# Kernel optimization log

Measured on AMD Instinct MI355X. Metric: run time of the kernel, lower is better.

Reference implementation:

```python
import jax, jax.numpy as jnp
import numpy as np

N, K, A, LOCAL, PAIR = 1024, 48, 5, 512, 128
RBF_BINS = 16

def _normalize(v, eps=1e-8):
    return v / jnp.sqrt(jnp.sum(v * v, axis=-1, keepdims=True) + eps)

def _frames(pos):
    # pos: (N, A, 3); backbone frame from N(0), CA(1), C(2) via Gram-Schmidt
    n, ca, c = pos[:, 0], pos[:, 1], pos[:, 2]
    e1 = _normalize(c - ca)
    v2 = n - ca
    e2 = _normalize(v2 - jnp.sum(v2 * e1, -1, keepdims=True) * e1)
    e3 = jnp.cross(e1, e2)
    R = jnp.stack([e1, e2, e3], axis=-1)  # (N,3,3) columns are frame axes
    return R, ca

def _rbf(d, d_min=0.0, d_max=22.0, bins=RBF_BINS):
    centers = jnp.linspace(d_min, d_max, bins)
    step = (d_max - d_min) / bins
    return jnp.exp(-((d[..., None] - centers) / step) ** 2)

def setup_inputs():
    key = jax.random.key(0)
    ks = jax.random.split(key, 16)
    def rn(k, shape, scale=1.0):
        return (scale * jax.random.normal(k, shape)).astype(jnp.float32)
    local = rn(ks[0], (N, LOCAL))
    pos = rn(ks[1], (N, A, 3), 3.0)
    pair = rn(ks[2], (N, N, PAIR), 0.1)
    neighbours = jax.random.randint(ks[3], (N, K), 0, N).astype(jnp.int32)
    mask = jnp.ones((N,), dtype=bool)
    d_dist = A * A * RBF_BINS   # 400
    d_dir = A * A * 3           # 75
    d_vec = 2 * A * 3           # 30
    s = lambda f: 1.0 / np.sqrt(f)
    return dict(
        local=local, pos=pos, pair=pair, neighbours=neighbours, mask=mask,
        W_li=rn(ks[4], (LOCAL, PAIR), s(LOCAL)),
        W_lj=rn(ks[5], (LOCAL, PAIR), s(LOCAL)),
        W_dist=rn(ks[6], (d_dist, PAIR), s(d_dist)),
        W_dir=rn(ks[7], (d_dir, PAIR), s(d_dir)),
        W_rot=rn(ks[8], (9, PAIR), s(9)),
        W_vec=rn(ks[9], (d_vec, PAIR), s(d_vec)),
        ln_scale=jnp.ones((PAIR,), jnp.float32),
        ln_bias=jnp.zeros((PAIR,), jnp.float32),
        mlp_w1=rn(ks[10], (PAIR, 2 * PAIR), s(PAIR)),
        mlp_b1=jnp.zeros((2 * PAIR,), jnp.float32),
        mlp_w2=rn(ks[11], (2 * PAIR, PAIR), s(2 * PAIR)),
        mlp_b2=jnp.zeros((PAIR,), jnp.float32),
    )

def reference(local, pos, pair, neighbours, mask,
              W_li, W_lj, W_dist, W_dir, W_rot, W_vec,
              ln_scale, ln_bias, mlp_w1, mlp_b1, mlp_w2, mlp_b2):
    n_idx = jnp.arange(neighbours.shape[0])
    pair_mask = (mask[:, None] & mask[neighbours]) & (neighbours != -1)
    p = pair[n_idx[:, None], neighbours]                      # (N,K,PAIR) gather
    R, t = _frames(pos)                                       # (N,3,3), (N,3)
    pos_nb = pos[neighbours]                                  # (N,K,A,3)
    # source / target node feature projections
    p = p + (local @ W_li)[:, None] + (local @ W_lj)[neighbours]
    # distance features: all atom-pair distances, RBF-encoded in [0, 22]
    off = pos[:, None, :, None, :] - pos_nb[:, :, None, :, :] # (N,K,A,A,3)
    dist = jnp.sqrt(jnp.sum(off * off, -1) + 1e-8)            # (N,K,A,A)
    p = p + _rbf(dist).reshape(*neighbours.shape, -1) @ W_dist
    # direction features: atom-pair offsets in the local frame, normalized
    off_local = jnp.einsum('nij,nkabi->nkabj', R, off)
    p = p + _normalize(off_local).reshape(*neighbours.shape, -1) @ W_dir
    # relative rotation features: R_i^T R_j, flattened
    R_rel = jnp.einsum('nai,nkaj->nkij', R, R[neighbours])
    p = p + R_rel.reshape(*neighbours.shape, 9) @ W_rot
    # pair vector features: self and neighbour atoms in the local frame (x0.1)
    x_self = jnp.einsum('nij,nai->naj', R, pos - t[:, None])            # (N,A,3)
    x_nb = jnp.einsum('nij,nkai->nkaj', R, pos_nb - t[:, None, None])   # (N,K,A,3)
    vec = jnp.concatenate(
        (0.1 * jnp.broadcast_to(x_self[:, None], x_nb.shape), 0.1 * x_nb),
        axis=-1).reshape(*neighbours.shape, -1)
    p = p + vec @ W_vec
    # LayerNorm (scale + offset)
    mu = jnp.mean(p, -1, keepdims=True)
    var = jnp.var(p, -1, keepdims=True)
    p = (p - mu) * jax.lax.rsqrt(var + 1e-5) * ln_scale + ln_bias
    # MLP: hidden 2*PAIR, gelu, linear out
    p = jax.nn.gelu(p @ mlp_w1 + mlp_b1) @ mlp_w2 + mlp_b2
    return p, pair_mask
```

## Files before the change

kernel.cpp:

```cpp
#include <hip/hip_runtime.h>
#include <hip/hip_bf16.h>
#include <math.h>

#define N 1024
#define K 48
#define A 5
#define LOCALD 512
#define PAIRD 128
#define ROWS 32
#define FEATK 544
#define SF_STRIDE_B 1152

#define WS_LI (N*9 + N*3 + N*15)
#define WS_LJ (WS_LI + N*128)
#define WCT_OFF 1159168u
#define W1T_OFF 1298432u
#define W2T_OFF 1363968u
#define PA_OFF  1429504u
#define WS_NEEDED (1429504ull + 49152ull*128*2)

typedef _Float16 half8 __attribute__((ext_vector_type(8)));
typedef float f32x16 __attribute__((ext_vector_type(16)));

__device__ __forceinline__ float gelu_fast(float x) {
    float u2 = 1.5957691216057308f * x * (1.0f + 0.044715f * x * x);
    float t = __expf(-u2);
    return x * __builtin_amdgcn_rcpf(1.0f + t);
}

__device__ __forceinline__ void frame_from(const float* __restrict__ P, float* __restrict__ R) {
    float e1x = P[6] - P[3], e1y = P[7] - P[4], e1z = P[8] - P[5];
    float inv1 = rsqrtf(e1x * e1x + e1y * e1y + e1z * e1z + 1e-8f);
    e1x *= inv1; e1y *= inv1; e1z *= inv1;
    float v2x = P[0] - P[3], v2y = P[1] - P[4], v2z = P[2] - P[5];
    float dp = v2x * e1x + v2y * e1y + v2z * e1z;
    float e2x = v2x - dp * e1x, e2y = v2y - dp * e1y, e2z = v2z - dp * e1z;
    float inv2 = rsqrtf(e2x * e2x + e2y * e2y + e2z * e2z + 1e-8f);
    e2x *= inv2; e2y *= inv2; e2z *= inv2;
    float e3x = e1y * e2z - e1z * e2y;
    float e3y = e1z * e2x - e1x * e2z;
    float e3z = e1x * e2y - e1y * e2x;
    R[0] = e1x; R[1] = e2x; R[2] = e3x;
    R[3] = e1y; R[4] = e2y; R[5] = e3y;
    R[6] = e1z; R[7] = e2z; R[8] = e3z;
}

__global__ __launch_bounds__(256) void prep_kernel(
    const float* __restrict__ local_,
    const float* __restrict__ W_li, const float* __restrict__ W_lj,
    const float* __restrict__ Wd, const float* __restrict__ Wdir,
    const float* __restrict__ Wrot, const float* __restrict__ Wv,
    const float* __restrict__ w1, const float* __restrict__ w2,
    float* __restrict__ ws, char* __restrict__ wsb)
{
    const int tid = threadIdx.x;
    if (blockIdx.x >= 256) {
        _Float16* wct = (_Float16*)(wsb + WCT_OFF);
        _Float16* w1t = (_Float16*)(wsb + W1T_OFF);
        _Float16* w2t = (_Float16*)(wsb + W2T_OFF);
        int g = (blockIdx.x - 256) * 256 + tid;
        if (g < 128 * 544) {
            int c = g & 127, f = g >> 7;
            float v = 0.0f;
            if (f < 400) v = Wd[(size_t)f * 128 + c];
            else if (f < 475) v = Wdir[(size_t)(f - 400) * 128 + c];
            else if (f < 484) v = Wrot[(size_t)(f - 475) * 128 + c];
            else if (f < 514) v = Wv[(size_t)(f - 484) * 128 + c];
            wct[(size_t)c * FEATK + f] = (_Float16)v;
        } else {
            int g2 = g - 128 * 544;
            if (g2 < 256 * 128) {
                int c = g2 & 255, f = g2 >> 8;
                w1t[(size_t)c * 128 + f] = (_Float16)w1[(size_t)f * 256 + c];
            } else {
                int g3 = g2 - 256 * 128;
                if (g3 < 128 * 256) {
                    int c = g3 & 127, f = g3 >> 7;
                    w2t[(size_t)c * 256 + f] = (_Float16)w2[(size_t)f * 128 + c];
                }
            }
        }
        return;
    }

    const int n0 = blockIdx.x * 4;
    __shared__ float sl[4][LOCALD];
    for (int t = tid; t < 4 * LOCALD; t += 256) {
        int r = t >> 9, q = t & 511;
        sl[r][q] = local_[(size_t)(n0 + r) * LOCALD + q];
    }
    __syncthreads();

    const int c = tid & 127;
    const int hh = tid >> 7;
    const int r0 = hh * 2;
    float ali0 = 0, ali1 = 0, alj0 = 0, alj1 = 0;
    const float* wli = W_li + c;
    const float* wlj = W_lj + c;
    #pragma unroll 8
    for (int f = 0; f < LOCALD; ++f) {
        float a_ = wli[(size_t)f * 128];
        float b_ = wlj[(size_t)f * 128];
        float l0 = sl[r0 + 0][f], l1 = sl[r0 + 1][f];
        ali0 += l0 * a_; ali1 += l1 * a_;
        alj0 += l0 * b_; alj1 += l1 * b_;
    }
    ws[WS_LI + (size_t)(n0 + r0 + 0) * 128 + c] = ali0;
    ws[WS_LI + (size_t)(n0 + r0 + 1) * 128 + c] = ali1;
    ws[WS_LJ + (size_t)(n0 + r0 + 0) * 128 + c] = alj0;
    ws[WS_LJ + (size_t)(n0 + r0 + 1) * 128 + c] = alj1;
}

__device__ __forceinline__ void sfw(char* smem, int r, int f, float v) {
    int off = r * SF_STRIDE_B + ((f * 2) ^ ((r & 7) << 4));
    *(_Float16*)(smem + off) = (_Float16)v;
}

template<bool SPLIT>
__global__ __launch_bounds__(256, 4) void main_kernel(
    const float* __restrict__ pair, const float* __restrict__ pos,
    const int* __restrict__ neigh, const int* __restrict__ mask,
    const float* __restrict__ ln_s, const float* __restrict__ ln_b,
    const float* __restrict__ b1, const float* __restrict__ b2,
    const float* __restrict__ ws, const char* __restrict__ wsb,
    _Float16* __restrict__ pa, float* __restrict__ out)
{
    const int R0 = blockIdx.x * ROWS;
    const int tid = threadIdx.x;
    const int lane = tid & 63;
    const int wv = tid >> 6;
    const int myrow = lane & 31;
    const int hi = lane >> 5;
    const int khalf = hi * 8;
    const int swz = (myrow & 7) << 4;

    __shared__ __align__(16) char smem[40960];
    int*   sn  = (int*)(smem + 36864);
    int*   sj  = (int*)(smem + 36992);
    float* spn = (float*)(smem + 37120);
    float* spj = (float*)(smem + 39040);

    const _Float16* wct = (const _Float16*)(wsb + WCT_OFF);
    const int colbase = wv * 32 + myrow;

    if (tid < ROWS) {
        int Rg = R0 + tid;
        int n = Rg / K;
        int kk = Rg - n * K;
        int j = neigh[n * K + kk];
        if (j < 0) j += N;
        sn[tid] = n; sj[tid] = j;
    }
    __syncthreads();

    const int nb0 = R0 / K;
    const int nb1 = (nb0 + 1 < N) ? nb0 + 1 : nb0;
    float li0 = ws[WS_LI + (size_t)nb0 * PAIRD + colbase];
    float li1 = ws[WS_LI + (size_t)nb1 * PAIRD + colbase];
    float pv[16];
    #pragma unroll
    for (int q = 0; q < 16; ++q) {
        int rr = (q & 3) + 8 * (q >> 2) + 4 * hi;
        int nq = sn[rr], jq = sj[rr];
        float li = (nq == nb0) ? li0 : li1;
        pv[q] = __builtin_nontemporal_load(&pair[((size_t)nq * N + jq) * PAIRD + colbase])
              + ws[WS_LJ + (size_t)jq * PAIRD + colbase] + li;
    }

    for (int t = tid; t < ROWS * 15; t += 256) {
        int r = t / 15, q = t % 15;
        spn[t] = pos[(size_t)sn[r] * 15 + q];
        spj[t] = pos[(size_t)sj[r] * 15 + q];
    }
    __syncthreads();

    {
        const int fr  = tid >> 3;
        const int sub = tid & 7;
        const float* Pn = spn + fr * 15;
        const float* Pj = spj + fr * 15;

        sfw(smem, fr, 514 + sub, 0.0f);
        sfw(smem, fr, 522 + sub, 0.0f);
        sfw(smem, fr, 530 + sub, 0.0f);
        if (sub < 6) sfw(smem, fr, 538 + sub, 0.0f);

        float rn[9];
        frame_from(Pn, rn);

        #pragma unroll
        for (int m = 0; m < 4; ++m) {
            int ab = sub + 8 * m;
            if (ab < 25) {
                int a = ab / 5, b = ab - 5 * (ab / 5);
                float o0 = Pn[a * 3 + 0] - Pj[b * 3 + 0];
                float o1 = Pn[a * 3 + 1] - Pj[b * 3 + 1];
                float o2 = Pn[a * 3 + 2] - Pj[b * 3 + 2];
                float d = sqrtf(o0 * o0 + o1 * o1 + o2 * o2 + 1e-8f);
                float z = d * (16.0f / 22.0f);
                int base = a * 80 + b * 16;
                int rb = fr * SF_STRIDE_B;
                int rsw = (fr & 7) << 4;
                #pragma unroll
                for (int bp = 0; bp < 8; ++bp) {
                    float e0 = __expf(-z * z);
                    float z1 = z - 1.0666666666666667f;
                    float e1 = __expf(-z1 * z1);
                    z = z1 - 1.0666666666666667f;
                    union { _Float16 h[2]; unsigned u; } pk;
                    pk.h[0] = (_Float16)e0; pk.h[1] = (_Float16)e1;
                    int off = rb + (((base + bp * 2) * 2) ^ rsw);
                    *(unsigned*)(smem + off) = pk.u;
                }
                float l0 = rn[0] * o0 + rn[3] * o1 + rn[6] * o2;
                float l1 = rn[1] * o0 + rn[4] * o1 + rn[7] * o2;
                float l2 = rn[2] * o0 + rn[5] * o1 + rn[8] * o2;
                float inv = rsqrtf(l0 * l0 + l1 * l1 + l2 * l2 + 1e-8f);
                int dbase = 400 + a * 15 + b * 3;
                sfw(smem, fr, dbase + 0, l0 * inv);
                sfw(smem, fr, dbase + 1, l1 * inv);
                sfw(smem, fr, dbase + 2, l2 * inv);
            }
        }

        #pragma unroll
        for (int m = 0; m < 2; ++m) {
            int task = (m == 0) ? sub : (sub < 2 ? 8 + sub : -1);
            if (task >= 0) {
                int a = task >> 1;
                int kind = task & 1;
                const float* Ps = kind ? Pj : Pn;
                float v0 = Ps[a * 3 + 0] - Pn[3];
                float v1 = Ps[a * 3 + 1] - Pn[4];
                float v2 = Ps[a * 3 + 2] - Pn[5];
                float x0 = rn[0] * v0 + rn[3] * v1 + rn[6] * v2;
                float x1 = rn[1] * v0 + rn[4] * v1 + rn[7] * v2;
                float x2 = rn[2] * v0 + rn[5] * v1 + rn[8] * v2;
                int dbase = 484 + a * 6 + kind * 3;
                sfw(smem, fr, dbase + 0, 0.1f * x0);
                sfw(smem, fr, dbase + 1, 0.1f * x1);
                sfw(smem, fr, dbase + 2, 0.1f * x2);
            }
        }

        if (sub == 7) {
            float rj[9];
            frame_from(Pj, rj);
            #pragma unroll
            for (int i = 0; i < 3; ++i)
                #pragma unroll
                for (int jd = 0; jd < 3; ++jd) {
                    float v = rn[0 * 3 + i] * rj[0 * 3 + jd]
                            + rn[1 * 3 + i] * rj[1 * 3 + jd]
                            + rn[2 * 3 + i] * rj[2 * 3 + jd];
                    sfw(smem, fr, 475 + i * 3 + jd, v);
                }
        }
    }
    __syncthreads();

    f32x16 acc0, acc1;
    #pragma unroll
    for (int q = 0; q < 16; ++q) { acc0[q] = 0.0f; acc1[q] = 0.0f; }
    {
        const _Float16* wp = wct + (size_t)colbase * FEATK + khalf;
        #pragma unroll
        for (int ks = 0; ks < 34; ks += 2) {
            half8 b0 = *(const half8*)(wp + ks * 16);
            half8 b1 = *(const half8*)(wp + (ks + 1) * 16);
            int k0 = ks * 16 + khalf;
            int k1 = (ks + 1) * 16 + khalf;
            half8 a0 = *(const half8*)(smem + myrow * SF_STRIDE_B + ((k0 * 2) ^ swz));
            half8 a1 = *(const half8*)(smem + myrow * SF_STRIDE_B + ((k1 * 2) ^ swz));
            acc0 = __builtin_amdgcn_mfma_f32_32x32x16_f16(a0, b0, acc0, 0, 0, 0);
            acc1 = __builtin_amdgcn_mfma_f32_32x32x16_f16(a1, b1, acc1, 0, 0, 0);
        }
    }
    __syncthreads();

    #pragma unroll
    for (int q = 0; q < 16; ++q) {
        int rr = (q & 3) + 8 * (q >> 2) + 4 * hi;
        *(float*)(smem + rr * 512 + colbase * 4) = acc0[q] + acc1[q] + pv[q];
    }
    __syncthreads();

    {
        float lns0 = ln_s[lane], lns1 = ln_s[lane + 64];
        float lnb0 = ln_b[lane], lnb1 = ln_b[lane + 64];
        #pragma unroll
        for (int rr8 = 0; rr8 < 8; ++rr8) {
            int row = wv * 8 + rr8;
            float v0 = *(float*)(smem + row * 512 + lane * 4);
            float v1 = *(float*)(smem + row * 512 + (lane + 64) * 4);
            float s = v0 + v1, s2 = v0 * v0 + v1 * v1;
            #pragma unroll
            for (int o = 32; o > 0; o >>= 1) {
                s += __shfl_xor(s, o, 64);
                s2 += __shfl_xor(s2, o, 64);
            }
            float mu = s * (1.0f / 128.0f);
            float var = s2 * (1.0f / 128.0f) - mu * mu;
            float rs = rsqrtf(var + 1e-5f);
            float y0 = (v0 - mu) * rs * lns0 + lnb0;
            float y1 = (v1 - mu) * rs * lns1 + lnb1;
            if constexpr (SPLIT) {
                pa[(size_t)(R0 + row) * PAIRD + lane]      = (_Float16)y0;
                pa[(size_t)(R0 + row) * PAIRD + lane + 64] = (_Float16)y1;
            } else {
                int sw = (row & 7) << 4;
                *(_Float16*)(smem + 16384 + row * 256 + ((lane * 2) ^ sw)) = (_Float16)y0;
                *(_Float16*)(smem + 16384 + row * 256 + (((lane + 64) * 2) ^ sw)) = (_Float16)y1;
            }
        }
    }
    if constexpr (SPLIT) return;

    __syncthreads();

    {
        const _Float16* w1t = (const _Float16*)(wsb + W1T_OFF);
        const int c0 = wv * 64 + myrow;
        const int c1 = c0 + 32;
        const _Float16* wp0 = w1t + (size_t)c0 * 128 + khalf;
        const _Float16* wp1 = w1t + (size_t)c1 * 128 + khalf;
        f32x16 h0, h1;
        #pragma unroll
        for (int q = 0; q < 16; ++q) { h0[q] = 0.0f; h1[q] = 0.0f; }
        #pragma unroll
        for (int ks = 0; ks < 8; ++ks) {
            half8 wf0 = *(const half8*)(wp0 + ks * 16);
            half8 wf1 = *(const half8*)(wp1 + ks * 16);
            int k0 = ks * 16 + khalf;
            half8 a = *(const half8*)(smem + 16384 + myrow * 256 + ((k0 * 2) ^ swz));
            h0 = __builtin_amdgcn_mfma_f32_32x32x16_f16(a, wf0, h0, 0, 0, 0);
            h1 = __builtin_amdgcn_mfma_f32_32x32x16_f16(a, wf1, h1, 0, 0, 0);
        }
        float bb0 = b1[c0], bb1 = b1[c1];
        #pragma unroll
        for (int q = 0; q < 16; ++q) {
            int rr = (q & 3) + 8 * (q >> 2) + 4 * hi;
            int sw = (rr & 7) << 4;
            *(_Float16*)(smem + rr * 512 + ((c0 * 2) ^ sw)) = (_Float16)gelu_fast(h0[q] + bb0);
            *(_Float16*)(smem + rr * 512 + ((c1 * 2) ^ sw)) = (_Float16)gelu_fast(h1[q] + bb1);
        }
    }
    __syncthreads();

    {
        const _Float16* w2t = (const _Float16*)(wsb + W2T_OFF);
        const int oc = wv * 32 + myrow;
        const _Float16* wp = w2t + (size_t)oc * 256 + khalf;
        f32x16 o0, o1;
        #pragma unroll
        for (int q = 0; q < 16; ++q) { o0[q] = 0.0f; o1[q] = 0.0f; }
        #pragma unroll
        for (int ks = 0; ks < 16; ks += 2) {
            half8 w0 = *(const half8*)(wp + ks * 16);
            half8 w1f = *(const half8*)(wp + (ks + 1) * 16);
            int k0 = ks * 16 + khalf;
            int k1 = (ks + 1) * 16 + khalf;
            half8 a0 = *(const half8*)(smem + myrow * 512 + ((k0 * 2) ^ swz));
            half8 a1 = *(const half8*)(smem + myrow * 512 + ((k1 * 2) ^ swz));
            o0 = __builtin_amdgcn_mfma_f32_32x32x16_f16(a0, w0, o0, 0, 0, 0);
            o1 = __builtin_amdgcn_mfma_f32_32x32x16_f16(a1, w1f, o1, 0, 0, 0);
        }
        float bb = b2[oc];
        #pragma unroll
        for (int q = 0; q < 16; ++q) {
            int rr = (q & 3) + 8 * (q >> 2) + 4 * hi;
            __builtin_nontemporal_store(o0[q] + o1[q] + bb,
                &out[((size_t)(R0 + rr)) * PAIRD + oc]);
        }
    }

    if (tid < ROWS) {
        int Rg = R0 + tid;
        int n = Rg / K;
        int kk = Rg - n * K;
        int jr = neigh[n * K + kk];
        int jj = jr < 0 ? jr + N : jr;
        bool pm = (jr != -1) && (mask[n] != 0) && (mask[jj] != 0);
        out[(size_t)N * K * PAIRD + Rg] = pm ? 1.0f : 0.0f;
    }
}

__global__ __launch_bounds__(256, 3) void mlp_kernel(
    const _Float16* __restrict__ pa, const int* __restrict__ neigh,
    const int* __restrict__ mask, const float* __restrict__ b1,
    const float* __restrict__ b2, const char* __restrict__ wsb,
    float* __restrict__ out)
{
    const int R0 = blockIdx.x * 64;
    const int tid = threadIdx.x;
    const int lane = tid & 63;
    const int wv = tid >> 6;
    const int myrow = lane & 31;
    const int hi = lane >> 5;
    const int khalf = hi * 8;
    const int swz = (myrow & 7) << 4;

    __shared__ __align__(16) char smem[49152];

    for (int ch = tid; ch < 1024; ch += 256) {
        int row = ch >> 4, c16 = ch & 15;
        half8 v = *(const half8*)(pa + (size_t)(R0 + row) * PAIRD + c16 * 8);
        *(half8*)(smem + row * 256 + ((c16 * 16) ^ ((row & 7) << 4))) = v;
    }
    __syncthreads();

    {
        const _Float16* w1t = (const _Float16*)(wsb + W1T_OFF);
        const int c0 = wv * 64 + myrow;
        const int c1 = c0 + 32;
        const _Float16* wp0 = w1t + (size_t)c0 * 128 + khalf;
        const _Float16* wp1 = w1t + (size_t)c1 * 128 + khalf;
        f32x16 h00, h01, h10, h11;
        #pragma unroll
        for (int q = 0; q < 16; ++q) { h00[q] = 0.0f; h01[q] = 0.0f; h10[q] = 0.0f; h11[q] = 0.0f; }
        #pragma unroll
        for (int ks = 0; ks < 8; ++ks) {
            int k0 = ks * 16 + khalf;
            half8 wf0 = *(const half8*)(wp0 + ks * 16);
            half8 wf1 = *(const half8*)(wp1 + ks * 16);
            half8 a0 = *(const half8*)(smem + myrow * 256 + ((k0 * 2) ^ swz));
            half8 a1 = *(const half8*)(smem + (32 + myrow) * 256 + ((k0 * 2) ^ swz));
            h00 = __builtin_amdgcn_mfma_f32_32x32x16_f16(a0, wf0, h00, 0, 0, 0);
            h01 = __builtin_amdgcn_mfma_f32_32x32x16_f16(a0, wf1, h01, 0, 0, 0);
            h10 = __builtin_amdgcn_mfma_f32_32x32x16_f16(a1, wf0, h10, 0, 0, 0);
            h11 = __builtin_amdgcn_mfma_f32_32x32x16_f16(a1, wf1, h11, 0, 0, 0);
        }
        float bb0 = b1[c0], bb1 = b1[c1];
        #pragma unroll
        for (int q = 0; q < 16; ++q) {
            int rr = (q & 3) + 8 * (q >> 2) + 4 * hi;
            int sw = (rr & 7) << 4;
            *(_Float16*)(smem + 16384 + rr * 512 + ((c0 * 2) ^ sw)) = (_Float16)gelu_fast(h00[q] + bb0);
            *(_Float16*)(smem + 16384 + rr * 512 + ((c1 * 2) ^ sw)) = (_Float16)gelu_fast(h01[q] + bb1);
            *(_Float16*)(smem + 16384 + (rr + 32) * 512 + ((c0 * 2) ^ sw)) = (_Float16)gelu_fast(h10[q] + bb0);
            *(_Float16*)(smem + 16384 + (rr + 32) * 512 + ((c1 * 2) ^ sw)) = (_Float16)gelu_fast(h11[q] + bb1);
        }
    }
    __syncthreads();

    {
        const _Float16* w2t = (const _Float16*)(wsb + W2T_OFF);
        const int oc = wv * 32 + myrow;
        const _Float16* wp = w2t + (size_t)oc * 256 + khalf;
        f32x16 o0, o1;
        #pragma unroll
        for (int q = 0; q < 16; ++q) { o0[q] = 0.0f; o1[q] = 0.0f; }
        #pragma unroll
        for (int ks = 0; ks < 16; ++ks) {
            int k0 = ks * 16 + khalf;
            half8 wf = *(const half8*)(wp + ks * 16);
            half8 a0 = *(const half8*)(smem + 16384 + myrow * 512 + ((k0 * 2) ^ swz));
            half8 a1 = *(const half8*)(smem + 16384 + (32 + myrow) * 512 + ((k0 * 2) ^ swz));
            o0 = __builtin_amdgcn_mfma_f32_32x32x16_f16(a0, wf, o0, 0, 0, 0);
            o1 = __builtin_amdgcn_mfma_f32_32x32x16_f16(a1, wf, o1, 0, 0, 0);
        }
        float bb = b2[oc];
        #pragma unroll
        for (int q = 0; q < 16; ++q) {
            int rr = (q & 3) + 8 * (q >> 2) + 4 * hi;
            __builtin_nontemporal_store(o0[q] + bb, &out[((size_t)(R0 + rr)) * PAIRD + oc]);
            __builtin_nontemporal_store(o1[q] + bb, &out[((size_t)(R0 + rr + 32)) * PAIRD + oc]);
        }
    }

    if (tid < 64) {
        int Rg = R0 + tid;
        int n = Rg / K;
        int kk = Rg - n * K;
        int jr = neigh[n * K + kk];
        int jj = jr < 0 ? jr + N : jr;
        bool pm = (jr != -1) && (mask[n] != 0) && (mask[jj] != 0);
        out[(size_t)N * K * PAIRD + Rg] = pm ? 1.0f : 0.0f;
    }
}

extern "C" void kernel_launch(void* const* d_in, const int* in_sizes, int n_in,
                              void* d_out, int out_size, void* d_ws, size_t ws_size,
                              hipStream_t stream) {
    const float* local_ = (const float*)d_in[0];
    const float* pos = (const float*)d_in[1];
    const float* pair = (const float*)d_in[2];
    const int* neigh = (const int*)d_in[3];
    const int* mask = (const int*)d_in[4];
    const float* W_li = (const float*)d_in[5];
    const float* W_lj = (const float*)d_in[6];
    const float* W_dist = (const float*)d_in[7];
    const float* W_dir = (const float*)d_in[8];
    const float* W_rot = (const float*)d_in[9];
    const float* W_vec = (const float*)d_in[10];
    const float* ln_s = (const float*)d_in[11];
    const float* ln_b = (const float*)d_in[12];
    const float* w1 = (const float*)d_in[13];
    const float* b1 = (const float*)d_in[14];
    const float* w2 = (const float*)d_in[15];
    const float* b2 = (const float*)d_in[16];
    float* ws = (float*)d_ws;
    char* wsb = (char*)d_ws;
    _Float16* pa = (_Float16*)(wsb + PA_OFF);
    float* out = (float*)d_out;

    hipLaunchKernelGGL(prep_kernel, dim3(256 + 528), dim3(256), 0, stream,
                       local_, W_li, W_lj, W_dist, W_dir, W_rot, W_vec,
                       w1, w2, ws, wsb);
    if (ws_size >= WS_NEEDED) {
        main_kernel<true><<<dim3((N * K) / ROWS), dim3(256), 0, stream>>>(
            pair, pos, neigh, mask, ln_s, ln_b, b1, b2, ws, wsb, pa, out);
        mlp_kernel<<<dim3((N * K) / 64), dim3(256), 0, stream>>>(
            pa, neigh, mask, b1, b2, wsb, out);
    } else {
        main_kernel<false><<<dim3((N * K) / ROWS), dim3(256), 0, stream>>>(
            pair, pos, neigh, mask, ln_s, ln_b, b1, b2, ws, wsb, pa, out);
    }
}
```

Before: 79.72 us.

## Split feature GEMM into two K-halves to shrink LDS and raise occupancy

```diff
diff --git a/kernel.cpp b/kernel.cpp
--- a/kernel.cpp
+++ b/kernel.cpp
@@ -9,7 +9,7 @@
 #define PAIRD 128
 #define ROWS 32
 #define FEATK 544
-#define SF_STRIDE_B 1152
+#define SF_STRIDE_B 640
 
 #define WS_LI (N*9 + N*3 + N*15)
 #define WS_LJ (WS_LI + N*128)
@@ -117,7 +117,7 @@
 }
 
 template<bool SPLIT>
-__global__ __launch_bounds__(256, 4) void main_kernel(
+__global__ __launch_bounds__(256, 6) void main_kernel(
     const float* __restrict__ pair, const float* __restrict__ pos,
     const int* __restrict__ neigh, const int* __restrict__ mask,
     const float* __restrict__ ln_s, const float* __restrict__ ln_b,
@@ -134,11 +134,11 @@
     const int khalf = hi * 8;
     const int swz = (myrow & 7) << 4;
 
-    __shared__ __align__(16) char smem[40960];
-    int*   sn  = (int*)(smem + 36864);
-    int*   sj  = (int*)(smem + 36992);
-    float* spn = (float*)(smem + 37120);
-    float* spj = (float*)(smem + 39040);
+    __shared__ __align__(16) char smem[24576];
+    int*   sn  = (int*)(smem + 20480);
+    int*   sj  = (int*)(smem + 20608);
+    float* spn = (float*)(smem + 20736);
+    float* spj = (float*)(smem + 22656);
 
     const _Float16* wct = (const _Float16*)(wsb + WCT_OFF);
     const int colbase = wv * 32 + myrow;
@@ -174,31 +174,23 @@
     }
     __syncthreads();
 
-    {
-        const int fr  = tid >> 3;
-        const int sub = tid & 7;
-        const float* Pn = spn + fr * 15;
-        const float* Pj = spj + fr * 15;
-
-        sfw(smem, fr, 514 + sub, 0.0f);
-        sfw(smem, fr, 522 + sub, 0.0f);
-        sfw(smem, fr, 530 + sub, 0.0f);
-        if (sub < 6) sfw(smem, fr, 538 + sub, 0.0f);
-
-        float rn[9];
-        frame_from(Pn, rn);
-
-        #pragma unroll
-        for (int m = 0; m < 4; ++m) {
+    const int fr  = tid >> 3;
+    const int sub = tid & 7;
+    const float* Pn = spn + fr * 15;
+    const float* Pj = spj + fr * 15;
+
+    {
+        #pragma unroll
+        for (int m = 0; m < 3; ++m) {
             int ab = sub + 8 * m;
-            if (ab < 25) {
+            if (ab < 17) {
                 int a = ab / 5, b = ab - 5 * (ab / 5);
                 float o0 = Pn[a * 3 + 0] - Pj[b * 3 + 0];
                 float o1 = Pn[a * 3 + 1] - Pj[b * 3 + 1];
                 float o2 = Pn[a * 3 + 2] - Pj[b * 3 + 2];
                 float d = sqrtf(o0 * o0 + o1 * o1 + o2 * o2 + 1e-8f);
                 float z = d * (16.0f / 22.0f);
-                int base = a * 80 + b * 16;
+                int base = ab * 16;
                 int rb = fr * SF_STRIDE_B;
                 int rsw = (fr & 7) << 4;
                 #pragma unroll
@@ -212,17 +204,70 @@
                     int off = rb + (((base + bp * 2) * 2) ^ rsw);
                     *(unsigned*)(smem + off) = pk.u;
                 }
+            }
+        }
+    }
+    __syncthreads();
+
+    f32x16 acc;
+    #pragma unroll
+    for (int q = 0; q < 16; ++q) acc[q] = 0.0f;
+    {
+        const _Float16* wp = wct + (size_t)colbase * FEATK + khalf;
+        #pragma unroll
+        for (int ks = 0; ks < 17; ++ks) {
+            half8 b0 = *(const half8*)(wp + ks * 16);
+            int k0 = ks * 16 + khalf;
+            half8 a0 = *(const half8*)(smem + myrow * SF_STRIDE_B + ((k0 * 2) ^ swz));
+            acc = __builtin_amdgcn_mfma_f32_32x32x16_f16(a0, b0, acc, 0, 0, 0);
+        }
+    }
+    __syncthreads();
+
+    {
+        float rn[9];
+        frame_from(Pn, rn);
+        {
+            int ab = 17 + sub;
+            int a = ab / 5, b = ab - 5 * (ab / 5);
+            float o0 = Pn[a * 3 + 0] - Pj[b * 3 + 0];
+            float o1 = Pn[a * 3 + 1] - Pj[b * 3 + 1];
+            float o2 = Pn[a * 3 + 2] - Pj[b * 3 + 2];
+            float d = sqrtf(o0 * o0 + o1 * o1 + o2 * o2 + 1e-8f);
+            float z = d * (16.0f / 22.0f);
+            int base = sub * 16;
+            int rb = fr * SF_STRIDE_B;
+            int rsw = (fr & 7) << 4;
+            #pragma unroll
+            for (int bp = 0; bp < 8; ++bp) {
+                float e0 = __expf(-z * z);
+                float z1 = z - 1.0666666666666667f;
+                float e1 = __expf(-z1 * z1);
+                z = z1 - 1.0666666666666667f;
+                union { _Float16 h[2]; unsigned u; } pk;
+                pk.h[0] = (_Float16)e0; pk.h[1] = (_Float16)e1;
+                int off = rb + (((base + bp * 2) * 2) ^ rsw);
+                *(unsigned*)(smem + off) = pk.u;
+            }
+        }
+        #pragma unroll
+        for (int m = 0; m < 4; ++m) {
+            int ab = sub + 8 * m;
+            if (ab < 25) {
+                int a = ab / 5, b = ab - 5 * (ab / 5);
+                float o0 = Pn[a * 3 + 0] - Pj[b * 3 + 0];
+                float o1 = Pn[a * 3 + 1] - Pj[b * 3 + 1];
+                float o2 = Pn[a * 3 + 2] - Pj[b * 3 + 2];
                 float l0 = rn[0] * o0 + rn[3] * o1 + rn[6] * o2;
                 float l1 = rn[1] * o0 + rn[4] * o1 + rn[7] * o2;
                 float l2 = rn[2] * o0 + rn[5] * o1 + rn[8] * o2;
                 float inv = rsqrtf(l0 * l0 + l1 * l1 + l2 * l2 + 1e-8f);
-                int dbase = 400 + a * 15 + b * 3;
+                int dbase = 128 + ab * 3;
                 sfw(smem, fr, dbase + 0, l0 * inv);
                 sfw(smem, fr, dbase + 1, l1 * inv);
                 sfw(smem, fr, dbase + 2, l2 * inv);
             }
         }
-
         #pragma unroll
         for (int m = 0; m < 2; ++m) {
             int task = (m == 0) ? sub : (sub < 2 ? 8 + sub : -1);
@@ -236,13 +281,12 @@
                 float x0 = rn[0] * v0 + rn[3] * v1 + rn[6] * v2;
                 float x1 = rn[1] * v0 + rn[4] * v1 + rn[7] * v2;
                 float x2 = rn[2] * v0 + rn[5] * v1 + rn[8] * v2;
-                int dbase = 484 + a * 6 + kind * 3;
+                int dbase = 212 + a * 6 + kind * 3;
                 sfw(smem, fr, dbase + 0, 0.1f * x0);
                 sfw(smem, fr, dbase + 1, 0.1f * x1);
                 sfw(smem, fr, dbase + 2, 0.1f * x2);
             }
         }
-
         if (sub == 7) {
             float rj[9];
             frame_from(Pj, rj);
@@ -253,27 +297,23 @@
                     float v = rn[0 * 3 + i] * rj[0 * 3 + jd]
                             + rn[1 * 3 + i] * rj[1 * 3 + jd]
                             + rn[2 * 3 + i] * rj[2 * 3 + jd];
-                    sfw(smem, fr, 475 + i * 3 + jd, v);
+                    sfw(smem, fr, 203 + i * 3 + jd, v);
                 }
-        }
-    }
-    __syncthreads();
-
-    f32x16 acc0, acc1;
-    #pragma unroll
-    for (int q = 0; q < 16; ++q) { acc0[q] = 0.0f; acc1[q] = 0.0f; }
-    {
-        const _Float16* wp = wct + (size_t)colbase * FEATK + khalf;
-        #pragma unroll
-        for (int ks = 0; ks < 34; ks += 2) {
-            half8 b0 = *(const half8*)(wp + ks * 16);
-            half8 b1 = *(const half8*)(wp + (ks + 1) * 16);
+        } else {
+            sfw(smem, fr, 242 + sub * 2 + 0, 0.0f);
+            sfw(smem, fr, 242 + sub * 2 + 1, 0.0f);
+        }
+    }
+    __syncthreads();
+
+    {
+        const _Float16* wpB = wct + (size_t)colbase * FEATK + khalf + 272;
+        #pragma unroll
+        for (int ks = 0; ks < 16; ++ks) {
+            half8 b0 = *(const half8*)(wpB + ks * 16);
             int k0 = ks * 16 + khalf;
-            int k1 = (ks + 1) * 16 + khalf;
             half8 a0 = *(const half8*)(smem + myrow * SF_STRIDE_B + ((k0 * 2) ^ swz));
-            half8 a1 = *(const half8*)(smem + myrow * SF_STRIDE_B + ((k1 * 2) ^ swz));
-            acc0 = __builtin_amdgcn_mfma_f32_32x32x16_f16(a0, b0, acc0, 0, 0, 0);
-            acc1 = __builtin_amdgcn_mfma_f32_32x32x16_f16(a1, b1, acc1, 0, 0, 0);
+            acc = __builtin_amdgcn_mfma_f32_32x32x16_f16(a0, b0, acc, 0, 0, 0);
         }
     }
     __syncthreads();
@@ -281,7 +321,7 @@
     #pragma unroll
     for (int q = 0; q < 16; ++q) {
         int rr = (q & 3) + 8 * (q >> 2) + 4 * hi;
-        *(float*)(smem + rr * 512 + colbase * 4) = acc0[q] + acc1[q] + pv[q];
+        *(float*)(smem + rr * 512 + colbase * 4) = acc[q] + pv[q];
     }
     __syncthreads();
 
```

New measurement: 115.5 us. +44.9%, slower.
